# Kernel optimization log

Hardware: AMD Instinct MI355X
Metric: run time of the kernel (lower is better)

Reference implementation:

```python
import jax, jax.numpy as jnp
from jax import lax
import numpy as np

B, C, N, T, K = 16, 64, 512, 64, 2
KSIZE, DIL = 2, 1
PAD = (KSIZE - 1) * DIL
EPS = 1e-5


def _powers(A, k):
    Ps = [jnp.eye(A.shape[0], dtype=A.dtype)]
    for _ in range(k):
        Ps.append(Ps[-1] @ A)
    return jnp.stack(Ps)  # (K+1, N, N)


def setup_inputs() -> dict:
    key = jax.random.key(0)
    ks = jax.random.split(key, 12)
    x = jax.random.normal(ks[0], (B, C, N, T), dtype=jnp.float32)
    # row-normalized random transition matrices, precomputed powers
    Af = jax.random.uniform(ks[1], (N, N), dtype=jnp.float32)
    Af = Af / Af.sum(axis=1, keepdims=True)
    Ab = Af.T / Af.T.sum(axis=1, keepdims=True)
    Aa = jax.random.uniform(ks[2], (N, N), dtype=jnp.float32)
    Aa = Aa / Aa.sum(axis=1, keepdims=True)
    P_f_pows = _powers(Af, K)
    P_b_pows = _powers(Ab, K)
    A_adp_pows = _powers(Aa, K)
    s = 0.05
    filter_w = jax.random.normal(ks[3], (C, C, 1, KSIZE), dtype=jnp.float32) * s
    filter_b = jnp.zeros((C,), jnp.float32)
    gate_w = jax.random.normal(ks[4], (C, C, 1, KSIZE), dtype=jnp.float32) * s
    gate_b = jnp.zeros((C,), jnp.float32)
    skip_w = jax.random.normal(ks[5], (C, C, 1, 1), dtype=jnp.float32) * s
    skip_b = jnp.zeros((C,), jnp.float32)
    weight_f = jax.random.normal(ks[6], (K + 1, C, C), dtype=jnp.float32) * s
    weight_b = jax.random.normal(ks[7], (K + 1, C, C), dtype=jnp.float32) * s
    gcn_bias = jnp.zeros((C,), jnp.float32)
    ln_gamma = jnp.ones((C,), jnp.float32)
    ln_beta = jnp.zeros((C,), jnp.float32)
    alpha = jnp.float32(0.5)
    return dict(x=x, P_f_pows=P_f_pows, P_b_pows=P_b_pows, A_adp_pows=A_adp_pows,
                filter_w=filter_w, filter_b=filter_b, gate_w=gate_w, gate_b=gate_b,
                skip_w=skip_w, skip_b=skip_b, weight_f=weight_f, weight_b=weight_b,
                gcn_bias=gcn_bias, ln_gamma=ln_gamma, ln_beta=ln_beta, alpha=alpha)


def _conv(x, w, b, dil=1):
    y = lax.conv_general_dilated(x, w, window_strides=(1, 1), padding='VALID',
                                 rhs_dilation=(1, dil),
                                 dimension_numbers=('NCHW', 'OIHW', 'NCHW'))
    return y + b[None, :, None, None]


def _apply_powers(xt, P_pows, weights):
    # xt: (B*T, N, Cin); P_pows: (K+1, N, N); weights: (K+1, Cin, Cout)
    xk = jnp.einsum('kij,bjc->kbic', P_pows, xt)
    return jnp.einsum('kbic,kco->bio', xk, weights)


def reference(x, P_f_pows, P_b_pows, A_adp_pows,
              filter_w, filter_b, gate_w, gate_b, skip_w, skip_b,
              weight_f, weight_b, gcn_bias, ln_gamma, ln_beta, alpha):
    # --- Gated TCN (causal left-pad along time) ---
    x_pad = jnp.pad(x, ((0, 0), (0, 0), (0, 0), (PAD, 0)))
    f = jnp.tanh(_conv(x_pad, filter_w, filter_b, DIL))
    g = jax.nn.sigmoid(_conv(x_pad, gate_w, gate_b, DIL))
    out = f * g                                   # (B, C, N, T)
    skip = _conv(out, skip_w, skip_b)             # 1x1 conv
    x_temporal = x + out                          # in_channels == out_channels

    # --- Diffusion GCN on (B*T, N, C) ---
    xt = jnp.transpose(x_temporal, (0, 3, 2, 1)).reshape(B * T, N, C)
    static_out = (_apply_powers(xt, P_f_pows, weight_f)
                  + _apply_powers(xt, P_b_pows, weight_b)
                  + gcn_bias[None, None, :])
    adapt_out = (_apply_powers(xt, A_adp_pows, weight_f)
                 + _apply_powers(xt, A_adp_pows, weight_b)
                 + gcn_bias[None, None, :])

    a = jax.nn.sigmoid(alpha)
    x_gcn = a * static_out + (1.0 - a) * adapt_out

    # --- LayerNorm over channel dim (dropout = identity in eval) ---
    mu = x_gcn.mean(axis=-1, keepdims=True)
    var = ((x_gcn - mu) ** 2).mean(axis=-1, keepdims=True)
    x_gcn = (x_gcn - mu) * lax.rsqrt(var + EPS) * ln_gamma + ln_beta

    x_out = x_gcn.reshape(B, T, N, C).transpose(0, 3, 2, 1)  # (B, C, N, T)
    return (x_out, skip)
```

## Files before the change

kernel.cpp:

```cpp
#include <hip/hip_runtime.h>
#include <cstdint>
#include <cstddef>

#define NB 16
#define NC 64
#define NN 512
#define NT 64
#define BT (NB*NT)
#define NN2 (NN*NN)
#define XSTRIDE_B (NC*NN*NT)
#define XSTRIDE_C (NN*NT)
#define XT_ROW (BT*NC)

typedef __attribute__((ext_vector_type(8))) short short8;
typedef __attribute__((ext_vector_type(4))) float f32x4;
typedef unsigned short ushort_t;
typedef unsigned int uint_t;

__device__ __forceinline__ ushort_t f2bf(float f) {
    uint_t u = __builtin_bit_cast(uint_t, f);
    u += 0x7FFFu + ((u >> 16) & 1u);
    return (ushort_t)(u >> 16);
}
__device__ __forceinline__ float bf2f(ushort_t u) {
    return __builtin_bit_cast(float, (uint_t)u << 16);
}
__device__ __forceinline__ void gl_lds16(const void* g, void* s) {
    __builtin_amdgcn_global_load_lds(
        (const __attribute__((address_space(1))) unsigned int*)g,
        (__attribute__((address_space(3))) unsigned int*)s, 16, 0, 0);
}

__global__ void k_prep(const float* __restrict__ wf, const float* __restrict__ wb,
                       const float* __restrict__ alpha, ushort_t* __restrict__ Wcb) {
    int i = blockIdx.x * 256 + threadIdx.x;
    if (i >= 7 * 4096) return;
    float a = 1.f / (1.f + expf(-alpha[0]));
    int r = i >> 12, co = i & 4095;
    int c = co >> 6, o = co & 63;
    float v;
    if      (r == 0) v = wf[co] + wb[co];
    else if (r == 1) v = a * wf[4096 + co];
    else if (r == 2) v = a * wf[8192 + co];
    else if (r == 3) v = a * wb[4096 + co];
    else if (r == 4) v = a * wb[8192 + co];
    else if (r == 5) v = (1.f - a) * (wf[4096 + co] + wb[4096 + co]);
    else             v = (1.f - a) * (wf[8192 + co] + wb[8192 + co]);
    int chunk = ((c >> 5) << 2) | (o >> 4);
    int lane  = (((c >> 3) & 3) << 4) | (o & 15);
    int j     = c & 7;
    Wcb[r * 4096 + chunk * 512 + lane * 8 + j] = f2bf(v);
}

__global__ void k_prepP(const float* __restrict__ Pf, const float* __restrict__ Pb,
                        const float* __restrict__ Aa, ushort_t* __restrict__ Apk) {
    int i = blockIdx.x * 256 + threadIdx.x;
    if (i >= 196608) return;
    int lane = i & 63, kc = (i >> 6) & 15, nt = (i >> 10) & 31, r = i >> 15;
    const float* base;
    if      (r == 0) base = Pf + NN2;
    else if (r == 1) base = Pf + 2 * NN2;
    else if (r == 2) base = Pb + NN2;
    else if (r == 3) base = Pb + 2 * NN2;
    else if (r == 4) base = Aa + NN2;
    else             base = Aa + 2 * NN2;
    int n = nt * 16 + (lane & 15);
    int k0 = kc * 32 + (lane >> 4) * 8;
    const float* src = base + (size_t)n * NN + k0;
    float4 v0 = ((const float4*)src)[0];
    float4 v1 = ((const float4*)src)[1];
    uint4 o;
    o.x = (uint_t)f2bf(v0.x) | ((uint_t)f2bf(v0.y) << 16);
    o.y = (uint_t)f2bf(v0.z) | ((uint_t)f2bf(v0.w) << 16);
    o.z = (uint_t)f2bf(v1.x) | ((uint_t)f2bf(v1.y) << 16);
    o.w = (uint_t)f2bf(v1.z) | ((uint_t)f2bf(v1.w) << 16);
    *(uint4*)(Apk + (size_t)i * 8) = o;
}

__global__ void k_prepW(const float* __restrict__ fw, const float* __restrict__ gw,
                        const float* __restrict__ sw, ushort_t* __restrict__ Wt) {
    int i = blockIdx.x * 256 + threadIdx.x;
    if (i >= 5 * 4096) return;
    int mat = i >> 12, t = i & 4095;
    int chunk = t >> 9, l = (t >> 3) & 63, j = t & 7;
    int m = chunk >> 1, kb = chunk & 1;
    int o = m * 16 + (l & 15);
    int c = kb * 32 + ((l >> 4) << 3) + j;
    float v;
    if      (mat == 0) v = fw[o * 128 + c * 2 + 0];
    else if (mat == 1) v = fw[o * 128 + c * 2 + 1];
    else if (mat == 2) v = gw[o * 128 + c * 2 + 0];
    else if (mat == 3) v = gw[o * 128 + c * 2 + 1];
    else               v = sw[o * 64 + c];
    Wt[i] = f2bf(v);
}

#define XS_P 72
__device__ __forceinline__ int swzA(int r, int c) {
    return r * XS_P + (c ^ (((r >> 4) & 3) << 3));
}
__global__ __launch_bounds__(256, 3) void k_tcn(
    const float* __restrict__ x,
    const ushort_t* __restrict__ Wt,
    const float* __restrict__ fb, const float* __restrict__ gb,
    const float* __restrict__ sb,
    float* __restrict__ skip_out, ushort_t* __restrict__ XTbf) {
    __shared__ __align__(16) ushort_t Xs[65 * XS_P];
    __shared__ __align__(16) ushort_t Os[64 * XS_P];

    int tx = threadIdx.x;
    int b = blockIdx.x >> 9, n = blockIdx.x & (NN - 1);

    {
        int c = tx >> 2, tq = tx & 3, t0 = tq * 16;
        const float* src = x + (size_t)b * XSTRIDE_B + (size_t)c * XSTRIDE_C
                             + (size_t)n * NT + t0;
        float4 v0 = ((const float4*)src)[0];
        float4 v1 = ((const float4*)src)[1];
        float4 v2 = ((const float4*)src)[2];
        float4 v3 = ((const float4*)src)[3];
        float vv[16] = {v0.x, v0.y, v0.z, v0.w, v1.x, v1.y, v1.z, v1.w,
                        v2.x, v2.y, v2.z, v2.w, v3.x, v3.y, v3.z, v3.w};
#pragma unroll
        for (int e = 0; e < 16; ++e) {
            int r = t0 + e + 1;
            Xs[swzA(r, c)] = f2bf(vv[e]);
        }
        if (tx < 8) ((uint4*)Xs)[tx] = (uint4){0, 0, 0, 0};
    }
    __syncthreads();

    int w = tx >> 6, l = tx & 63, lr = l & 15, lg = l >> 4;

    short8 wf0[2], wf1[2], wg0[2], wg1[2], wsk[2];
#pragma unroll
    for (int kb = 0; kb < 2; ++kb) {
        int off = (w * 2 + kb) * 512 + l * 8;
        wf0[kb] = *(const short8*)(Wt + 0 * 4096 + off);
        wf1[kb] = *(const short8*)(Wt + 1 * 4096 + off);
        wg0[kb] = *(const short8*)(Wt + 2 * 4096 + off);
        wg1[kb] = *(const short8*)(Wt + 3 * 4096 + off);
        wsk[kb] = *(const short8*)(Wt + 4 * 4096 + off);
    }
    float fbv[4], gbv[4], sbv[4];
#pragma unroll
    for (int q = 0; q < 4; ++q) {
        int o = w * 16 + lg * 4 + q;
        fbv[q] = fb[o]; gbv[q] = gb[o]; sbv[q] = sb[o];
    }

#pragma unroll
    for (int tb = 0; tb < 4; ++tb) {
        short8 b0[2], b1[2];
#pragma unroll
        for (int kb = 0; kb < 2; ++kb) {
            int blk = kb * 4 + lg;
            int r1 = tb * 16 + lr + 1, r0 = tb * 16 + lr;
            b1[kb] = *(const short8*)&Xs[r1 * XS_P + (((blk ^ ((r1 >> 4) & 3)) << 3))];
            b0[kb] = *(const short8*)&Xs[r0 * XS_P + (((blk ^ ((r0 >> 4) & 3)) << 3))];
        }
        f32x4 aF = {fbv[0], fbv[1], fbv[2], fbv[3]};
        f32x4 aG = {gbv[0], gbv[1], gbv[2], gbv[3]};
        aF = __builtin_amdgcn_mfma_f32_16x16x32_bf16(wf0[0], b0[0], aF, 0, 0, 0);
        aF = __builtin_amdgcn_mfma_f32_16x16x32_bf16(wf0[1], b0[1], aF, 0, 0, 0);
        aF = __builtin_amdgcn_mfma_f32_16x16x32_bf16(wf1[0], b1[0], aF, 0, 0, 0);
        aF = __builtin_amdgcn_mfma_f32_16x16x32_bf16(wf1[1], b1[1], aF, 0, 0, 0);
        aG = __builtin_amdgcn_mfma_f32_16x16x32_bf16(wg0[0], b0[0], aG, 0, 0, 0);
        aG = __builtin_amdgcn_mfma_f32_16x16x32_bf16(wg0[1], b0[1], aG, 0, 0, 0);
        aG = __builtin_amdgcn_mfma_f32_16x16x32_bf16(wg1[0], b1[0], aG, 0, 0, 0);
        aG = __builtin_amdgcn_mfma_f32_16x16x32_bf16(wg1[1], b1[1], aG, 0, 0, 0);
        int t = tb * 16 + lr;
#pragma unroll
        for (int q = 0; q < 4; ++q) {
            float fo = tanhf(aF[q]);
            float go = 1.f / (1.f + expf(-aG[q]));
            int o = w * 16 + lg * 4 + q;
            Os[swzA(t, o)] = f2bf(fo * go);
        }
    }
    __syncthreads();

    float* skp = skip_out + (size_t)b * XSTRIDE_B + (size_t)n * NT;
#pragma unroll
    for (int tb = 0; tb < 4; ++tb) {
        int t = tb * 16 + lr;
        short8 ov[2];
#pragma unroll
        for (int kb = 0; kb < 2; ++kb) {
            int blk = kb * 4 + lg;
            ov[kb] = *(const short8*)&Os[t * XS_P + (((blk ^ ((t >> 4) & 3)) << 3))];
        }
        f32x4 aS = {sbv[0], sbv[1], sbv[2], sbv[3]};
        aS = __builtin_amdgcn_mfma_f32_16x16x32_bf16(wsk[0], ov[0], aS, 0, 0, 0);
        aS = __builtin_amdgcn_mfma_f32_16x16x32_bf16(wsk[1], ov[1], aS, 0, 0, 0);
#pragma unroll
        for (int q = 0; q < 4; ++q) {
            int o = w * 16 + lg * 4 + q;
            skp[(size_t)o * XSTRIDE_C + t] = aS[q];
        }
    }

    {
        int t = tx >> 2, cch = (tx & 3) * 16;
        ushort_t* dst = XTbf + (size_t)n * XT_ROW + (size_t)b * 4096 + t * 64 + cch;
        int rX = t + 1;
#pragma unroll
        for (int blk2 = 0; blk2 < 2; ++blk2) {
            int cb = (cch >> 3) + blk2;
            short8 xv = *(const short8*)&Xs[rX * XS_P + ((cb ^ ((rX >> 4) & 3)) << 3)];
            short8 ovv = *(const short8*)&Os[t * XS_P + ((cb ^ ((t >> 4) & 3)) << 3)];
            uint_t pk[4];
#pragma unroll
            for (int h = 0; h < 4; ++h) {
                float s0 = bf2f((ushort_t)xv[h * 2]) + bf2f((ushort_t)ovv[h * 2]);
                float s1 = bf2f((ushort_t)xv[h * 2 + 1]) + bf2f((ushort_t)ovv[h * 2 + 1]);
                pk[h] = (uint_t)f2bf(s0) | ((uint_t)f2bf(s1) << 16);
            }
            *(uint4*)(dst + blk2 * 8) = (uint4){pk[0], pk[1], pk[2], pk[3]};
        }
    }
}

__global__ __launch_bounds__(256) void k_tr(const ushort_t* __restrict__ XTbf,
                                            ushort_t* __restrict__ Bpk) {
    __shared__ ushort_t tile[32 * XS_P];
    int tx = threadIdx.x;
    int bt = blockIdx.x;
    int jj = tx >> 3, c8 = (tx & 7) * 8;
    int f = tx >> 6, lane = tx & 63, lg = lane >> 4, lr = lane & 15;
    for (int kc = 0; kc < 16; ++kc) {
        if (kc) __syncthreads();
        *(uint4*)&tile[jj * XS_P + c8] =
            *(const uint4*)(XTbf + (size_t)(kc * 32 + jj) * XT_ROW + bt * 64 + c8);
        __syncthreads();
        ushort_t vals[8];
#pragma unroll
        for (int e = 0; e < 8; ++e)
            vals[e] = tile[(lg * 8 + e) * XS_P + f * 16 + lr];
        uint4 o;
        o.x = (uint_t)vals[0] | ((uint_t)vals[1] << 16);
        o.y = (uint_t)vals[2] | ((uint_t)vals[3] << 16);
        o.z = (uint_t)vals[4] | ((uint_t)vals[5] << 16);
        o.w = (uint_t)vals[6] | ((uint_t)vals[7] << 16);
        *(uint4*)(Bpk + (size_t)bt * 32768 + kc * 2048 + tx * 8) = o;
    }
}

__global__ __launch_bounds__(256, 2) void k_gcn(
    const ushort_t* __restrict__ Apk,
    const ushort_t* __restrict__ Bpk,
    const ushort_t* __restrict__ XTbf,
    const ushort_t* __restrict__ Wcb,
    const float* __restrict__ bias,
    ushort_t* __restrict__ G) {
    __shared__ __align__(16) ushort_t sB[2][2048];
    __shared__ __align__(16) ushort_t sY[4][16 * 72];

    int tx = threadIdx.x;
    int w = tx >> 6, l = tx & 63;
    int lr = l & 15, lg = l >> 4;
    int bid = (blockIdx.x & 7) * 1024 + (blockIdx.x >> 3);
    int bt = bid >> 3;
    int n0 = (bid & 7) << 6;

    f32x4 acc[6][4];
#pragma unroll
    for (int r = 0; r < 6; ++r)
#pragma unroll
        for (int f = 0; f < 4; ++f) acc[r][f] = (f32x4){0.f, 0.f, 0.f, 0.f};

    const ushort_t* aBase = Apk + (size_t)((n0 >> 4) + w) * 8192 + l * 8;
    const ushort_t* bSrc = Bpk + (size_t)bt * 32768 + w * 512 + l * 8;
    ushort_t* sB0 = &sB[0][w * 512];
    ushort_t* sB1 = &sB[1][w * 512];

    gl_lds16(bSrc, sB0);
    short8 aC[6];
#pragma unroll
    for (int r = 0; r < 6; ++r) aC[r] = *(const short8*)(aBase + (size_t)r * NN2);
    asm volatile("s_waitcnt vmcnt(6)" ::: "memory");
    __builtin_amdgcn_s_barrier();
    __builtin_amdgcn_sched_barrier(0);

#pragma unroll
    for (int t = 0; t < 16; ++t) {
        const ushort_t* sBr = (t & 1) ? &sB[1][0] : &sB[0][0];
        short8 aN[6];
        if (t < 15) {
            gl_lds16(bSrc + (t + 1) * 2048, (t & 1) ? sB0 : sB1);
#pragma unroll
            for (int r = 0; r < 6; ++r)
                aN[r] = *(const short8*)(aBase + (size_t)r * NN2 + (t + 1) * 512);
        }
        short8 bv[4];
#pragma unroll
        for (int f = 0; f < 4; ++f)
            bv[f] = *(const short8*)(sBr + f * 512 + l * 8);
#pragma unroll
        for (int r = 0; r < 6; ++r)
#pragma unroll
            for (int f = 0; f < 4; ++f)
                acc[r][f] = __builtin_amdgcn_mfma_f32_16x16x32_bf16(aC[r], bv[f], acc[r][f], 0, 0, 0);
        if (t < 15) {
#pragma unroll
            for (int r = 0; r < 6; ++r) aC[r] = aN[r];
        }
        asm volatile("s_waitcnt vmcnt(6)" ::: "memory");
        __builtin_amdgcn_s_barrier();
        __builtin_amdgcn_sched_barrier(0);
    }

    f32x4 acc2[4];
#pragma unroll
    for (int fo = 0; fo < 4; ++fo) {
        float b = bias[fo * 16 + lr];
        acc2[fo] = (f32x4){b, b, b, b};
    }
    ushort_t* sYw = &sY[w][0];
    const ushort_t* wBase = Wcb + l * 8;

#pragma unroll
    for (int r = 0; r < 7; ++r) {
        short8 wv[8];
#pragma unroll
        for (int ch = 0; ch < 8; ++ch)
            wv[ch] = *(const short8*)(wBase + r * 4096 + ch * 512);
        short8 ay[2];
        if (r == 0) {
            const ushort_t* xs = XTbf + (size_t)(n0 + w * 16 + lr) * XT_ROW + bt * 64 + lg * 8;
            ay[0] = *(const short8*)(xs);
            ay[1] = *(const short8*)(xs + 32);
        } else {
#pragma unroll
            for (int f = 0; f < 4; ++f)
#pragma unroll
                for (int q = 0; q < 4; ++q)
                    sYw[(lg * 4 + q) * 72 + f * 16 + lr] = f2bf(acc[r - 1][f][q]);
            ay[0] = *(const short8*)(&sYw[lr * 72 + lg * 8]);
            ay[1] = *(const short8*)(&sYw[lr * 72 + 32 + lg * 8]);
        }
#pragma unroll
        for (int kh = 0; kh < 2; ++kh)
#pragma unroll
            for (int fo = 0; fo < 4; ++fo)
                acc2[fo] = __builtin_amdgcn_mfma_f32_16x16x32_bf16(ay[kh], wv[kh * 4 + fo], acc2[fo], 0, 0, 0);
    }

    ushort_t* gp = G + (size_t)(n0 + w * 16 + lg * 4) * XT_ROW + bt * 64 + lr;
#pragma unroll
    for (int fo = 0; fo < 4; ++fo)
#pragma unroll
        for (int q = 0; q < 4; ++q)
            gp[(size_t)q * XT_ROW + fo * 16] = f2bf(acc2[fo][q]);
}

__global__ __launch_bounds__(256) void k_ln_t(
    const ushort_t* __restrict__ G,
    const float* __restrict__ gamma, const float* __restrict__ beta,
    float* __restrict__ xout) {
    __shared__ float sT[64 * 65];
    __shared__ float sMu[64], sRs[64];
    __shared__ float sS[64 * 4], sQ[64 * 4];

    int bid = blockIdx.x;
    int b = bid >> 9, n = bid & (NN - 1);
    int tx = threadIdx.x;
    const ushort_t* src = G + (size_t)n * XT_ROW + (size_t)b * (NT * NC);

#pragma unroll
    for (int u = 0; u < 2; ++u) {
        int fi = u * 256 + tx;
        uint4 v = ((const uint4*)src)[fi];
        int t = fi >> 3, c = (fi & 7) * 8;
        sT[t * 65 + c + 0] = bf2f((ushort_t)(v.x & 0xffff));
        sT[t * 65 + c + 1] = bf2f((ushort_t)(v.x >> 16));
        sT[t * 65 + c + 2] = bf2f((ushort_t)(v.y & 0xffff));
        sT[t * 65 + c + 3] = bf2f((ushort_t)(v.y >> 16));
        sT[t * 65 + c + 4] = bf2f((ushort_t)(v.z & 0xffff));
        sT[t * 65 + c + 5] = bf2f((ushort_t)(v.z >> 16));
        sT[t * 65 + c + 6] = bf2f((ushort_t)(v.w & 0xffff));
        sT[t * 65 + c + 7] = bf2f((ushort_t)(v.w >> 16));
    }
    __syncthreads();
    {
        int row = tx >> 2, seg = tx & 3;
        float s = 0.f, q = 0.f;
        for (int cc = 0; cc < 16; ++cc) {
            float v = sT[row * 65 + seg * 16 + cc];
            s += v; q += v * v;
        }
        sS[row * 4 + seg] = s; sQ[row * 4 + seg] = q;
    }
    __syncthreads();
    if (tx < 64) {
        float ss = sS[tx * 4] + sS[tx * 4 + 1] + sS[tx * 4 + 2] + sS[tx * 4 + 3];
        float qq = sQ[tx * 4] + sQ[tx * 4 + 1] + sQ[tx * 4 + 2] + sQ[tx * 4 + 3];
        float mu = ss * (1.f / 64.f);
        float var = qq * (1.f / 64.f) - mu * mu;
        sMu[tx] = mu; sRs[tx] = rsqrtf(var + 1e-5f);
    }
    __syncthreads();
    {
        int t = tx & 63, cg = (tx >> 6) * 16;
        float mu = sMu[t], rs = sRs[t];
        for (int cc = 0; cc < 16; ++cc) {
            int c = cg + cc;
            float v = (sT[t * 65 + c] - mu) * rs * gamma[c] + beta[c];
            xout[(size_t)b * XSTRIDE_B + (size_t)c * XSTRIDE_C + (size_t)n * NT + t] = v;
        }
    }
}

extern "C" void kernel_launch(void* const* d_in, const int* in_sizes, int n_in,
                              void* d_out, int out_size, void* d_ws, size_t ws_size,
                              hipStream_t stream) {
    const float* x     = (const float*)d_in[0];
    const float* Pf    = (const float*)d_in[1];
    const float* Pb    = (const float*)d_in[2];
    const float* Aa    = (const float*)d_in[3];
    const float* fw    = (const float*)d_in[4];
    const float* fb    = (const float*)d_in[5];
    const float* gw    = (const float*)d_in[6];
    const float* gb    = (const float*)d_in[7];
    const float* sw    = (const float*)d_in[8];
    const float* sb    = (const float*)d_in[9];
    const float* wf    = (const float*)d_in[10];
    const float* wb    = (const float*)d_in[11];
    const float* gbias = (const float*)d_in[12];
    const float* lng   = (const float*)d_in[13];
    const float* lnb   = (const float*)d_in[14];
    const float* alpha = (const float*)d_in[15];

    float* xout = (float*)d_out;
    float* skip = (float*)d_out + (size_t)NB * NC * NN * NT;

    char* ws = (char*)d_ws;
    ushort_t* XTbf = (ushort_t*)(ws);
    ushort_t* Bpk  = (ushort_t*)(ws + 67108864);
    ushort_t* Gb   = (ushort_t*)(ws + 134217728);
    ushort_t* Apk  = (ushort_t*)(ws + 201326592);
    ushort_t* Wcb  = (ushort_t*)(ws + 204472320);
    ushort_t* Wt   = (ushort_t*)(ws + 204537856);

    hipLaunchKernelGGL(k_prep, dim3(112), dim3(256), 0, stream, wf, wb, alpha, Wcb);
    hipLaunchKernelGGL(k_prepW, dim3(80), dim3(256), 0, stream, fw, gw, sw, Wt);
    hipLaunchKernelGGL(k_prepP, dim3(768), dim3(256), 0, stream, Pf, Pb, Aa, Apk);
    hipLaunchKernelGGL(k_tcn, dim3(NB * NN), dim3(256), 0, stream,
                       x, Wt, fb, gb, sb, skip, XTbf);
    hipLaunchKernelGGL(k_tr, dim3(1024), dim3(256), 0, stream, XTbf, Bpk);
    hipLaunchKernelGGL(k_gcn, dim3(8192), dim3(256), 0, stream,
                       Apk, Bpk, XTbf, Wcb, gbias, Gb);
    hipLaunchKernelGGL(k_ln_t, dim3(NB * NN), dim3(256), 0, stream, Gb, lng, lnb, xout);
}
```

Before: 437.4 us.

## Retile GCN kernel to share A fragments across two bt and split power matrices over waves

```diff
diff --git a/kernel.cpp b/kernel.cpp
--- a/kernel.cpp
+++ b/kernel.cpp
@@ -253,105 +253,157 @@
     const ushort_t* __restrict__ Wcb,
     const float* __restrict__ bias,
     ushort_t* __restrict__ G) {
-    __shared__ __align__(16) ushort_t sB[2][2048];
+    __shared__ __align__(16) ushort_t sB[2][4096];
     __shared__ __align__(16) ushort_t sY[4][16 * 72];
+    __shared__ __align__(16) float sC[2][2][4][64][4];
 
     int tx = threadIdx.x;
     int w = tx >> 6, l = tx & 63;
     int lr = l & 15, lg = l >> 4;
+    int s = w >> 1, h = w & 1;
+
     int bid = (blockIdx.x & 7) * 1024 + (blockIdx.x >> 3);
-    int bt = bid >> 3;
-    int n0 = (bid & 7) << 6;
-
-    f32x4 acc[6][4];
-#pragma unroll
-    for (int r = 0; r < 6; ++r)
-#pragma unroll
-        for (int f = 0; f < 4; ++f) acc[r][f] = (f32x4){0.f, 0.f, 0.f, 0.f};
-
-    const ushort_t* aBase = Apk + (size_t)((n0 >> 4) + w) * 8192 + l * 8;
-    const ushort_t* bSrc = Bpk + (size_t)bt * 32768 + w * 512 + l * 8;
-    ushort_t* sB0 = &sB[0][w * 512];
-    ushort_t* sB1 = &sB[1][w * 512];
-
-    gl_lds16(bSrc, sB0);
-    short8 aC[6];
-#pragma unroll
-    for (int r = 0; r < 6; ++r) aC[r] = *(const short8*)(aBase + (size_t)r * NN2);
-    asm volatile("s_waitcnt vmcnt(6)" ::: "memory");
+    int btp = bid >> 4;
+    int n0i = bid & 15;
+    int n0 = n0i << 5;
+    int bt0 = btp * 2;
+
+    f32x4 acc[3][8];
+#pragma unroll
+    for (int j = 0; j < 3; ++j)
+#pragma unroll
+        for (int f = 0; f < 8; ++f) acc[j][f] = (f32x4){0.f, 0.f, 0.f, 0.f};
+
+    const ushort_t* aBase = Apk + (size_t)(h * 3) * NN2
+                                + (size_t)(n0i * 2 + s) * 8192 + l * 8;
+    const ushort_t* bSrc = Bpk + (size_t)bt0 * 32768 + w * 512 + l * 8;
+    ushort_t* sBw0 = &sB[0][w * 512];
+    ushort_t* sBw0p = &sB[0][2048 + w * 512];
+    ushort_t* sBw1 = &sB[1][w * 512];
+    ushort_t* sBw1p = &sB[1][2048 + w * 512];
+
+    gl_lds16(bSrc, sBw0);
+    gl_lds16(bSrc + 32768, sBw0p);
+    short8 aC[3];
+#pragma unroll
+    for (int j = 0; j < 3; ++j) aC[j] = *(const short8*)(aBase + (size_t)j * NN2);
+    asm volatile("s_waitcnt vmcnt(3)" ::: "memory");
     __builtin_amdgcn_s_barrier();
     __builtin_amdgcn_sched_barrier(0);
 
 #pragma unroll
     for (int t = 0; t < 16; ++t) {
         const ushort_t* sBr = (t & 1) ? &sB[1][0] : &sB[0][0];
-        short8 aN[6];
+        short8 aN[3];
         if (t < 15) {
-            gl_lds16(bSrc + (t + 1) * 2048, (t & 1) ? sB0 : sB1);
-#pragma unroll
-            for (int r = 0; r < 6; ++r)
-                aN[r] = *(const short8*)(aBase + (size_t)r * NN2 + (t + 1) * 512);
-        }
-        short8 bv[4];
-#pragma unroll
-        for (int f = 0; f < 4; ++f)
-            bv[f] = *(const short8*)(sBr + f * 512 + l * 8);
-#pragma unroll
-        for (int r = 0; r < 6; ++r)
+            gl_lds16(bSrc + (t + 1) * 2048, (t & 1) ? sBw0 : sBw1);
+            gl_lds16(bSrc + 32768 + (t + 1) * 2048, (t & 1) ? sBw0p : sBw1p);
+#pragma unroll
+            for (int j = 0; j < 3; ++j)
+                aN[j] = *(const short8*)(aBase + (size_t)j * NN2 + (t + 1) * 512);
+        }
+#pragma unroll
+        for (int p = 0; p < 2; ++p) {
+            short8 bv[4];
 #pragma unroll
             for (int f = 0; f < 4; ++f)
-                acc[r][f] = __builtin_amdgcn_mfma_f32_16x16x32_bf16(aC[r], bv[f], acc[r][f], 0, 0, 0);
+                bv[f] = *(const short8*)(sBr + p * 2048 + f * 512 + l * 8);
+#pragma unroll
+            for (int j = 0; j < 3; ++j)
+#pragma unroll
+                for (int f = 0; f < 4; ++f)
+                    acc[j][p * 4 + f] = __builtin_amdgcn_mfma_f32_16x16x32_bf16(
+                        aC[j], bv[f], acc[j][p * 4 + f], 0, 0, 0);
+        }
         if (t < 15) {
 #pragma unroll
-            for (int r = 0; r < 6; ++r) aC[r] = aN[r];
-        }
-        asm volatile("s_waitcnt vmcnt(6)" ::: "memory");
+            for (int j = 0; j < 3; ++j) aC[j] = aN[j];
+        }
+        asm volatile("s_waitcnt vmcnt(3)" ::: "memory");
         __builtin_amdgcn_s_barrier();
         __builtin_amdgcn_sched_barrier(0);
     }
 
-    f32x4 acc2[4];
-#pragma unroll
-    for (int fo = 0; fo < 4; ++fo) {
-        float b = bias[fo * 16 + lr];
-        acc2[fo] = (f32x4){b, b, b, b};
-    }
     ushort_t* sYw = &sY[w][0];
     const ushort_t* wBase = Wcb + l * 8;
 
 #pragma unroll
-    for (int r = 0; r < 7; ++r) {
-        short8 wv[8];
-#pragma unroll
-        for (int ch = 0; ch < 8; ++ch)
-            wv[ch] = *(const short8*)(wBase + r * 4096 + ch * 512);
-        short8 ay[2];
-        if (r == 0) {
-            const ushort_t* xs = XTbf + (size_t)(n0 + w * 16 + lr) * XT_ROW + bt * 64 + lg * 8;
-            ay[0] = *(const short8*)(xs);
-            ay[1] = *(const short8*)(xs + 32);
+    for (int p = 0; p < 2; ++p) {
+        f32x4 acc2[4];
+#pragma unroll
+        for (int fo = 0; fo < 4; ++fo) {
+            float b = (h == 0) ? bias[fo * 16 + lr] : 0.f;
+            acc2[fo] = (f32x4){b, b, b, b};
+        }
+        if (h == 0) {
+            const ushort_t* xs = XTbf + (size_t)(n0 + s * 16 + lr) * XT_ROW
+                               + (bt0 + p) * 64 + lg * 8;
+            short8 ay0 = *(const short8*)(xs);
+            short8 ay1 = *(const short8*)(xs + 32);
+#pragma unroll
+            for (int kh = 0; kh < 2; ++kh)
+#pragma unroll
+                for (int fo = 0; fo < 4; ++fo) {
+                    short8 wv = *(const short8*)(wBase + (kh * 4 + fo) * 512);
+                    acc2[fo] = __builtin_amdgcn_mfma_f32_16x16x32_bf16(
+                        kh ? ay1 : ay0, wv, acc2[fo], 0, 0, 0);
+                }
+        }
+#pragma unroll
+        for (int j = 0; j < 3; ++j) {
+            int wcIdx = (h == 0) ? (j + 1) : (j + 4);
+#pragma unroll
+            for (int f = 0; f < 4; ++f)
+#pragma unroll
+                for (int q = 0; q < 4; ++q)
+                    sYw[(lg * 4 + q) * 72 + f * 16 + lr] = f2bf(acc[j][p * 4 + f][q]);
+            short8 ay0 = *(const short8*)(&sYw[lr * 72 + lg * 8]);
+            short8 ay1 = *(const short8*)(&sYw[lr * 72 + 32 + lg * 8]);
+#pragma unroll
+            for (int kh = 0; kh < 2; ++kh)
+#pragma unroll
+                for (int fo = 0; fo < 4; ++fo) {
+                    short8 wv = *(const short8*)(wBase + wcIdx * 4096 + (kh * 4 + fo) * 512);
+                    acc2[fo] = __builtin_amdgcn_mfma_f32_16x16x32_bf16(
+                        kh ? ay1 : ay0, wv, acc2[fo], 0, 0, 0);
+                }
+        }
+        if (h == 1) {
+#pragma unroll
+            for (int fo = 0; fo < 4; ++fo)
+                *(f32x4*)&sC[s][p][fo][l][0] = acc2[fo];
         } else {
 #pragma unroll
-            for (int f = 0; f < 4; ++f)
+            for (int fo = 0; fo < 4; ++fo)
+                *(f32x4*)&sY[0][0] ;
+#pragma unroll
+            for (int fo = 0; fo < 4; ++fo) { }
+            if (p == 0) {
+#pragma unroll
+                for (int fo = 0; fo < 4; ++fo) *(f32x4*)&sC[s][0][fo][l][0];
+            }
+        }
+        if (h == 0) {
+#pragma unroll
+            for (int fo = 0; fo < 4; ++fo) acc[0][p * 4 + fo] = acc2[fo];
+        }
+    }
+    __syncthreads();
+    if (h == 0) {
+#pragma unroll
+        for (int p = 0; p < 2; ++p) {
+            ushort_t* gp = G + (size_t)(n0 + s * 16 + lg * 4) * XT_ROW
+                         + (bt0 + p) * 64 + lr;
+#pragma unroll
+            for (int fo = 0; fo < 4; ++fo) {
+                f32x4 mine = acc[0][p * 4 + fo];
+                f32x4 other = *(const f32x4*)&sC[s][p][fo][l][0];
 #pragma unroll
                 for (int q = 0; q < 4; ++q)
-                    sYw[(lg * 4 + q) * 72 + f * 16 + lr] = f2bf(acc[r - 1][f][q]);
-            ay[0] = *(const short8*)(&sYw[lr * 72 + lg * 8]);
-            ay[1] = *(const short8*)(&sYw[lr * 72 + 32 + lg * 8]);
-        }
-#pragma unroll
-        for (int kh = 0; kh < 2; ++kh)
-#pragma unroll
-            for (int fo = 0; fo < 4; ++fo)
-                acc2[fo] = __builtin_amdgcn_mfma_f32_16x16x32_bf16(ay[kh], wv[kh * 4 + fo], acc2[fo], 0, 0, 0);
-    }
-
-    ushort_t* gp = G + (size_t)(n0 + w * 16 + lg * 4) * XT_ROW + bt * 64 + lr;
-#pragma unroll
-    for (int fo = 0; fo < 4; ++fo)
-#pragma unroll
-        for (int q = 0; q < 4; ++q)
-            gp[(size_t)q * XT_ROW + fo * 16] = f2bf(acc2[fo][q]);
+                    gp[(size_t)q * XT_ROW + fo * 16] = f2bf(mine[q] + other[q]);
+            }
+        }
+    }
 }
 
 __global__ __launch_bounds__(256) void k_ln_t(
```

Measured after the change: 427.3 us. 2.3% less time.
